# Kernel optimization log

Hardware: AMD Instinct MI355X
Metric: run time of the kernel (lower is better)

The kernel has to match this reference:

```python
import jax, jax.numpy as jnp
import numpy as np

BITS = 4
PACK = 32 // BITS  # 8 nibbles per int32
GROUPSIZE = 128
IN_F, OUT_F = 4096, 11008
N_GROUPS = IN_F // GROUPSIZE


def setup_inputs() -> dict:
    key = jax.random.key(0)
    k1, k2, k3, k4, k5 = jax.random.split(key, 5)
    x = jax.random.normal(k1, (8192, IN_F), dtype=jnp.float32)
    # packed int4 weights: 8 values per int32 along the infeatures axis
    qweight = jax.random.randint(k2, (IN_F // PACK, OUT_F), jnp.iinfo(jnp.int32).min,
                                 jnp.iinfo(jnp.int32).max, dtype=jnp.int32)
    # packed int4 zero points: 8 values per int32 along the outfeatures axis
    qzeros = jax.random.randint(k3, (N_GROUPS, OUT_F // PACK), jnp.iinfo(jnp.int32).min,
                                jnp.iinfo(jnp.int32).max, dtype=jnp.int32)
    # small positive per-group scales, as produced by GPTQ quantization
    scales = (jax.random.uniform(k4, (N_GROUPS, OUT_F), dtype=jnp.float32) * 0.01 + 0.001)
    g_idx = (jnp.arange(IN_F, dtype=jnp.int32) // GROUPSIZE).astype(jnp.int32)
    bias = jax.random.normal(k5, (OUT_F,), dtype=jnp.float32)
    return {"x": x, "qweight": qweight, "qzeros": qzeros, "scales": scales,
            "g_idx": g_idx, "bias": bias}


def _unpack_int4_rows(packed):
    # packed: [in/8, out] int32 -> [in, out] int32 nibbles
    shifts = (BITS * jnp.arange(PACK, dtype=jnp.int32))  # [8]
    nib = (packed[:, None, :] >> shifts[None, :, None]) & 0xF  # [in/8, 8, out]
    return nib.reshape(packed.shape[0] * PACK, packed.shape[1])


def _unpack_int4_cols(packed):
    # packed: [G, out/8] int32 -> [G, out] int32 nibbles
    shifts = (BITS * jnp.arange(PACK, dtype=jnp.int32))  # [8]
    nib = (packed[:, :, None] >> shifts[None, None, :]) & 0xF  # [G, out/8, 8]
    return nib.reshape(packed.shape[0], packed.shape[1] * PACK)


def reference(x, qweight, qzeros, scales, g_idx, bias):
    q = _unpack_int4_rows(qweight)            # [in, out] int4 values in [0,15]
    z = _unpack_int4_cols(qzeros) + 1         # pack() stored zeros-1; GPTQ dequant adds it back
    # per-input-channel group lookup via g_idx
    s = scales[g_idx]                         # [in, out]
    zf = z[g_idx].astype(jnp.float32)         # [in, out]
    w = (q.astype(jnp.float32) - zf) * s      # dequantized weight [in, out]
    out = jnp.matmul(x, w) + bias             # [tokens, out]
    return out
```

## Files before the change

### kernel.cpp

```cpp
#include <hip/hip_runtime.h>
#include <stdint.h>

#define TOKENS 8192
#define IN_F   4096
#define OUT_F  11008
#define GROUPSIZE 128

#define BM 256
#define BN 256
#define BK 64
#define NT  (IN_F / BK)
#define NBM (TOKENS / BM)
#define NBN (OUT_F / BN)
#define NWG (NBM * NBN)

typedef __attribute__((ext_vector_type(8)))  short          bf16x8;
typedef __attribute__((ext_vector_type(4)))  float          f32x4;
typedef __attribute__((ext_vector_type(8)))  unsigned short u16x8;
typedef __attribute__((ext_vector_type(16))) unsigned short u16x16;

static __device__ __forceinline__ unsigned short f2bf(float f) {
    union { float f; unsigned int u; } v; v.f = f;
    unsigned int u = v.u;
    u += 0x7fffu + ((u >> 16) & 1u);
    return (unsigned short)(u >> 16);
}

__global__ void cvt_x_kernel(const float* __restrict__ x,
                             unsigned short* __restrict__ xb) {
    int i = (blockIdx.x * 256 + threadIdx.x) * 8;
    const float4* p = (const float4*)(x + i);
    float4 a = p[0];
    float4 b = p[1];
    u16x8 o;
    o[0] = f2bf(a.x); o[1] = f2bf(a.y); o[2] = f2bf(a.z); o[3] = f2bf(a.w);
    o[4] = f2bf(b.x); o[5] = f2bf(b.y); o[6] = f2bf(b.z); o[7] = f2bf(b.w);
    *(u16x8*)(xb + i) = o;
}

__global__ void dequant_kernel(const int* __restrict__ qweight,
                               const int* __restrict__ qzeros,
                               const float* __restrict__ scales,
                               unsigned short* __restrict__ Wt) {
    const int t   = threadIdx.x;
    const int n   = blockIdx.x * 32 + (t >> 3);
    const int kp0 = blockIdx.y * 16 + (t & 7) * 2;
    const int g   = blockIdx.y;
    const float s  = scales[g * OUT_F + n];
    const int   zq = ((qzeros[g * (OUT_F / 8) + (n >> 3)] >> (4 * (n & 7))) & 0xF) + 1;
    const float zs = (float)zq * s;
    const int qw0 = qweight[(size_t)kp0 * OUT_F + n];
    const int qw1 = qweight[(size_t)(kp0 + 1) * OUT_F + n];
    u16x16 o;
#pragma unroll
    for (int j = 0; j < 8; ++j) {
        o[j]     = f2bf(fmaf((float)((qw0 >> (4 * j)) & 0xF), s, -zs));
        o[j + 8] = f2bf(fmaf((float)((qw1 >> (4 * j)) & 0xF), s, -zs));
    }
    *(u16x16*)(Wt + (size_t)n * IN_F + kp0 * 8) = o;
}

#define GLD16(gp, lp)                                                        \
    __builtin_amdgcn_global_load_lds(                                        \
        (const __attribute__((address_space(1))) unsigned int*)(gp),         \
        (__attribute__((address_space(3))) unsigned int*)(lp), 16, 0, 0)

#define BARRIER() do {                                                       \
    asm volatile("" ::: "memory");                                           \
    __builtin_amdgcn_s_barrier();                                            \
    asm volatile("" ::: "memory");                                           \
} while (0)

#define LGKM0() do {                                                         \
    asm volatile("s_waitcnt lgkmcnt(0)" ::: "memory");                       \
    __builtin_amdgcn_sched_barrier(0);                                       \
} while (0)

__global__ __launch_bounds__(512, 2) void gemm_bias_kernel(
    const unsigned short* __restrict__ A,
    const unsigned short* __restrict__ Bt,
    const float* __restrict__ bias,
    float* __restrict__ C) {
    extern __shared__ char smem_c[];

    const int tid = threadIdx.x;
    const int l   = tid & 63;
    const int w   = tid >> 6;
    const int wr  = w >> 2;
    const int wc  = w & 3;

    const int bid = blockIdx.x;
    const int swz = (bid & 7) * (NWG / 8) + (bid >> 3);
    const int m0  = (swz / NBN) * BM;
    const int n0  = (swz % NBN) * BN;

    const int sperm = ((l & 7) ^ (l >> 3)) * 8;
    const unsigned short* aG = A  + (size_t)(m0 + w * 16 + (l >> 3)) * IN_F + sperm;
    const unsigned short* bG = Bt + (size_t)(n0 + w * 16 + (l >> 3)) * IN_F + sperm;
    char* sA = smem_c + w * 2048 + l * 16;
    char* sB = sA + 32768;

#define STAGE_A(b, h, tt) do {                                               \
    GLD16(aG + (size_t)((h) * 128    ) * IN_F + (tt) * 64,                   \
          sA + (b) * 65536 + (h) * 16384);                                   \
    GLD16(aG + (size_t)((h) * 128 + 8) * IN_F + (tt) * 64,                   \
          sA + (b) * 65536 + (h) * 16384 + 1024);                            \
} while (0)
#define STAGE_B(b, h, tt) do {                                               \
    GLD16(bG + (size_t)((h) * 128    ) * IN_F + (tt) * 64,                   \
          sB + (b) * 65536 + (h) * 16384);                                   \
    GLD16(bG + (size_t)((h) * 128 + 8) * IN_F + (tt) * 64,                   \
          sB + (b) * 65536 + (h) * 16384 + 1024);                            \
} while (0)

    const unsigned short* LAe = (const unsigned short*)smem_c;
    const unsigned short* LBe = (const unsigned short*)(smem_c + 32768);
    const int c0   = (((l >> 4) ^ (l & 7)) * 8);
    const int c1   = c0 ^ 32;
    const int arow = (wr * 128 + (l & 15)) * 64;
    const int brow = (wc * 64  + (l & 15)) * 64;

    f32x4  acc[8][4] = {};
    bf16x8 a0[2], a1[2], bfr[4][2];

#define RDA_PAIR(p, mi) do {                                                 \
    a0[0] = *(const bf16x8*)&(p)[arow + (mi) * 1024 + c0];                   \
    a0[1] = *(const bf16x8*)&(p)[arow + (mi) * 1024 + c1];                   \
    a1[0] = *(const bf16x8*)&(p)[arow + ((mi) + 1) * 1024 + c0];             \
    a1[1] = *(const bf16x8*)&(p)[arow + ((mi) + 1) * 1024 + c1];             \
} while (0)
#define RDB(p, nj) do {                                                      \
    bfr[nj][0] = *(const bf16x8*)&(p)[brow + (nj) * 1024 + c0];              \
    bfr[nj][1] = *(const bf16x8*)&(p)[brow + (nj) * 1024 + c1];              \
} while (0)
#define MM0(mi, nj, ks)                                                      \
    acc[mi][nj] = __builtin_amdgcn_mfma_f32_16x16x32_bf16(                   \
        a0[ks], bfr[nj][ks], acc[mi][nj], 0, 0, 0)
#define MM1(mi, nj, ks)                                                      \
    acc[mi][nj] = __builtin_amdgcn_mfma_f32_16x16x32_bf16(                   \
        a1[ks], bfr[nj][ks], acc[mi][nj], 0, 0, 0)
#define QUADP(e) do {                                                        \
    __builtin_amdgcn_s_setprio(1);                                           \
    MM0(e,0,0); MM0(e,1,0); MM0(e,2,0); MM0(e,3,0);                          \
    MM1((e)+1,0,0); MM1((e)+1,1,0); MM1((e)+1,2,0); MM1((e)+1,3,0);          \
    MM0(e,0,1); MM0(e,1,1); MM0(e,2,1); MM0(e,3,1);                          \
    MM1((e)+1,0,1); MM1((e)+1,1,1); MM1((e)+1,2,1); MM1((e)+1,3,1);          \
    __builtin_amdgcn_s_setprio(0);                                           \
} while (0)

    STAGE_A(0, 0, 0); STAGE_A(0, 1, 0);
    STAGE_B(0, 0, 0); STAGE_B(0, 1, 0);
    STAGE_B(1, 0, 1); STAGE_B(1, 1, 1);
    asm volatile("s_waitcnt vmcnt(4)" ::: "memory");
    __builtin_amdgcn_sched_barrier(0);
    BARRIER();

    for (int t = 0; t < NT; ++t) {
        const int bt = t & 1;
        const int bo = bt ^ 1;
        const unsigned short* pA = LAe + bt * 32768;
        const unsigned short* pB = LBe + bt * 32768;

        RDB(pB, 0); RDB(pB, 1); RDB(pB, 2); RDB(pB, 3);
        RDA_PAIR(pA, 0);
        if (t + 1 < NT) STAGE_A(bo, 0, t + 1);
        BARRIER();
        LGKM0();
        QUADP(0);
        BARRIER();

        RDA_PAIR(pA, 2);
        if (t + 1 < NT) STAGE_A(bo, 1, t + 1);
        BARRIER();
        LGKM0();
        QUADP(2);
        BARRIER();

        RDA_PAIR(pA, 4);
        if (t + 2 < NT) STAGE_B(bt, 0, t + 2);
        BARRIER();
        LGKM0();
        QUADP(4);
        BARRIER();

        RDA_PAIR(pA, 6);
        if (t + 2 < NT) STAGE_B(bt, 1, t + 2);
        BARRIER();
        LGKM0();
        QUADP(6);
        if (t < NT - 2)
            asm volatile("s_waitcnt vmcnt(4)" ::: "memory");
        else if (t == NT - 2)
            asm volatile("s_waitcnt vmcnt(0)" ::: "memory");
        __builtin_amdgcn_sched_barrier(0);
        BARRIER();
    }

    const int col = l & 15;
    const int r0  = (l >> 4) * 4;
#pragma unroll
    for (int nj = 0; nj < 4; ++nj) {
        const int n = n0 + wc * 64 + nj * 16 + col;
        const float bv = bias[n];
#pragma unroll
        for (int mi = 0; mi < 8; ++mi) {
            const int m = m0 + wr * 128 + mi * 16 + r0;
#pragma unroll
            for (int r = 0; r < 4; ++r)
                C[(size_t)(m + r) * OUT_F + n] = acc[mi][nj][r] + bv;
        }
    }
}

__global__ __launch_bounds__(256) void fallback_kernel(
    const float* __restrict__ x, const int* __restrict__ qweight,
    const int* __restrict__ qzeros, const float* __restrict__ scales,
    const float* __restrict__ bias, float* __restrict__ C) {
    const int n = blockIdx.x * 16 + (threadIdx.x & 15);
    const int m = blockIdx.y * 16 + (threadIdx.x >> 4);
    float acc = 0.f;
    const float* xr = x + (size_t)m * IN_F;
    for (int g = 0; g < IN_F / GROUPSIZE; ++g) {
        const float s  = scales[g * OUT_F + n];
        const float zs = s * (float)(((qzeros[g * (OUT_F / 8) + (n >> 3)]
                                       >> (4 * (n & 7))) & 0xF) + 1);
        for (int kp = g * 16; kp < g * 16 + 16; ++kp) {
            const int qw = qweight[kp * OUT_F + n];
#pragma unroll
            for (int j = 0; j < 8; ++j) {
                const float w = fmaf((float)((qw >> (4 * j)) & 0xF), s, -zs);
                acc = fmaf(xr[kp * 8 + j], w, acc);
            }
        }
    }
    C[(size_t)m * OUT_F + n] = acc + bias[n];
}

extern "C" void kernel_launch(void* const* d_in, const int* in_sizes, int n_in,
                              void* d_out, int out_size, void* d_ws, size_t ws_size,
                              hipStream_t stream) {
    const float* x       = (const float*)d_in[0];
    const int*   qweight = (const int*)  d_in[1];
    const int*   qzeros  = (const int*)  d_in[2];
    const float* scales  = (const float*)d_in[3];
    const float* bias    = (const float*)d_in[5];
    float* out = (float*)d_out;

    const size_t xb_bytes = (size_t)TOKENS * IN_F * sizeof(unsigned short);
    const size_t wt_bytes = (size_t)OUT_F  * IN_F * sizeof(unsigned short);

    if (ws_size >= xb_bytes + wt_bytes) {
        static bool attr_done = false;
        if (!attr_done) {
            (void)hipFuncSetAttribute((const void*)gemm_bias_kernel,
                                      hipFuncAttributeMaxDynamicSharedMemorySize,
                                      131072);
            attr_done = true;
        }
        unsigned short* xb = (unsigned short*)d_ws;
        unsigned short* Wt = (unsigned short*)((char*)d_ws + xb_bytes);
        cvt_x_kernel<<<(TOKENS * IN_F) / (256 * 8), 256, 0, stream>>>(x, xb);
        dequant_kernel<<<dim3(OUT_F / 32, IN_F / 8 / 16), 256, 0, stream>>>(
            qweight, qzeros, scales, Wt);
        gemm_bias_kernel<<<NWG, 512, 131072, stream>>>(xb, Wt, bias, out);
    } else {
        fallback_kernel<<<dim3(OUT_F / 16, TOKENS / 16), 256, 0, stream>>>(
            x, qweight, qzeros, scales, bias, out);
    }
}
```

Measured before the change: 1.080 ms.

## Triple-buffer A tiles and restructure GEMM main loop with partial LDS waits

```diff
diff --git a/kernel.cpp b/kernel.cpp
--- a/kernel.cpp
+++ b/kernel.cpp
@@ -71,8 +71,8 @@
     asm volatile("" ::: "memory");                                           \
 } while (0)
 
-#define LGKM0() do {                                                         \
-    asm volatile("s_waitcnt lgkmcnt(0)" ::: "memory");                       \
+#define LGKM(n) do {                                                         \
+    asm volatile("s_waitcnt lgkmcnt(" #n ")" ::: "memory");                  \
     __builtin_amdgcn_sched_barrier(0);                                       \
 } while (0)
 
@@ -97,103 +97,95 @@
     const int sperm = ((l & 7) ^ (l >> 3)) * 8;
     const unsigned short* aG = A  + (size_t)(m0 + w * 16 + (l >> 3)) * IN_F + sperm;
     const unsigned short* bG = Bt + (size_t)(n0 + w * 16 + (l >> 3)) * IN_F + sperm;
-    char* sA = smem_c + w * 2048 + l * 16;
-    char* sB = sA + 32768;
-
-#define STAGE_A(b, h, tt) do {                                               \
-    GLD16(aG + (size_t)((h) * 128    ) * IN_F + (tt) * 64,                   \
-          sA + (b) * 65536 + (h) * 16384);                                   \
-    GLD16(aG + (size_t)((h) * 128 + 8) * IN_F + (tt) * 64,                   \
-          sA + (b) * 65536 + (h) * 16384 + 1024);                            \
-} while (0)
-#define STAGE_B(b, h, tt) do {                                               \
-    GLD16(bG + (size_t)((h) * 128    ) * IN_F + (tt) * 64,                   \
-          sB + (b) * 65536 + (h) * 16384);                                   \
-    GLD16(bG + (size_t)((h) * 128 + 8) * IN_F + (tt) * 64,                   \
-          sB + (b) * 65536 + (h) * 16384 + 1024);                            \
-} while (0)
-
-    const unsigned short* LAe = (const unsigned short*)smem_c;
-    const unsigned short* LBe = (const unsigned short*)(smem_c + 32768);
+    const int sOff = w * 2048 + l * 16;
+
+#define STAGE_A4(lbase, tt) do {                                             \
+    GLD16(aG + (size_t)(tt) * 64,                      (lbase) + sOff);      \
+    GLD16(aG + (size_t)8   * IN_F + (size_t)(tt) * 64, (lbase) + sOff + 1024);\
+    GLD16(aG + (size_t)128 * IN_F + (size_t)(tt) * 64, (lbase) + sOff + 16384);\
+    GLD16(aG + (size_t)136 * IN_F + (size_t)(tt) * 64, (lbase) + sOff + 16384 + 1024);\
+} while (0)
+#define STAGE_B4(lbase, tt) do {                                             \
+    GLD16(bG + (size_t)(tt) * 64,                      (lbase) + sOff);      \
+    GLD16(bG + (size_t)8   * IN_F + (size_t)(tt) * 64, (lbase) + sOff + 1024);\
+    GLD16(bG + (size_t)128 * IN_F + (size_t)(tt) * 64, (lbase) + sOff + 16384);\
+    GLD16(bG + (size_t)136 * IN_F + (size_t)(tt) * 64, (lbase) + sOff + 16384 + 1024);\
+} while (0)
+
     const int c0   = (((l >> 4) ^ (l & 7)) * 8);
     const int c1   = c0 ^ 32;
     const int arow = (wr * 128 + (l & 15)) * 64;
     const int brow = (wc * 64  + (l & 15)) * 64;
 
     f32x4  acc[8][4] = {};
-    bf16x8 a0[2], a1[2], bfr[4][2];
-
-#define RDA_PAIR(p, mi) do {                                                 \
-    a0[0] = *(const bf16x8*)&(p)[arow + (mi) * 1024 + c0];                   \
-    a0[1] = *(const bf16x8*)&(p)[arow + (mi) * 1024 + c1];                   \
-    a1[0] = *(const bf16x8*)&(p)[arow + ((mi) + 1) * 1024 + c0];             \
-    a1[1] = *(const bf16x8*)&(p)[arow + ((mi) + 1) * 1024 + c1];             \
-} while (0)
-#define RDB(p, nj) do {                                                      \
-    bfr[nj][0] = *(const bf16x8*)&(p)[brow + (nj) * 1024 + c0];              \
-    bfr[nj][1] = *(const bf16x8*)&(p)[brow + (nj) * 1024 + c1];              \
-} while (0)
-#define MM0(mi, nj, ks)                                                      \
+    bf16x8 aP0[2], aP1[2], aQ0[2], aQ1[2], bfr[4][2];
+
+#define RDB4(p) do {                                                         \
+    bfr[0][0] = *(const bf16x8*)&(p)[brow + 0 * 1024 + c0];                  \
+    bfr[0][1] = *(const bf16x8*)&(p)[brow + 0 * 1024 + c1];                  \
+    bfr[1][0] = *(const bf16x8*)&(p)[brow + 1 * 1024 + c0];                  \
+    bfr[1][1] = *(const bf16x8*)&(p)[brow + 1 * 1024 + c1];                  \
+    bfr[2][0] = *(const bf16x8*)&(p)[brow + 2 * 1024 + c0];                  \
+    bfr[2][1] = *(const bf16x8*)&(p)[brow + 2 * 1024 + c1];                  \
+    bfr[3][0] = *(const bf16x8*)&(p)[brow + 3 * 1024 + c0];                  \
+    bfr[3][1] = *(const bf16x8*)&(p)[brow + 3 * 1024 + c1];                  \
+} while (0)
+#define RDA2(p, mi, d0, d1) do {                                             \
+    d0[0] = *(const bf16x8*)&(p)[arow + (mi) * 1024 + c0];                   \
+    d0[1] = *(const bf16x8*)&(p)[arow + (mi) * 1024 + c1];                   \
+    d1[0] = *(const bf16x8*)&(p)[arow + ((mi) + 1) * 1024 + c0];             \
+    d1[1] = *(const bf16x8*)&(p)[arow + ((mi) + 1) * 1024 + c1];             \
+} while (0)
+#define MMX(Af, mi, nj, ks)                                                  \
     acc[mi][nj] = __builtin_amdgcn_mfma_f32_16x16x32_bf16(                   \
-        a0[ks], bfr[nj][ks], acc[mi][nj], 0, 0, 0)
-#define MM1(mi, nj, ks)                                                      \
-    acc[mi][nj] = __builtin_amdgcn_mfma_f32_16x16x32_bf16(                   \
-        a1[ks], bfr[nj][ks], acc[mi][nj], 0, 0, 0)
-#define QUADP(e) do {                                                        \
+        Af[ks], bfr[nj][ks], acc[mi][nj], 0, 0, 0)
+#define QUADX(A0, A1, e) do {                                                \
     __builtin_amdgcn_s_setprio(1);                                           \
-    MM0(e,0,0); MM0(e,1,0); MM0(e,2,0); MM0(e,3,0);                          \
-    MM1((e)+1,0,0); MM1((e)+1,1,0); MM1((e)+1,2,0); MM1((e)+1,3,0);          \
-    MM0(e,0,1); MM0(e,1,1); MM0(e,2,1); MM0(e,3,1);                          \
-    MM1((e)+1,0,1); MM1((e)+1,1,1); MM1((e)+1,2,1); MM1((e)+1,3,1);          \
+    MMX(A0, e, 0, 0); MMX(A0, e, 1, 0); MMX(A0, e, 2, 0); MMX(A0, e, 3, 0);  \
+    MMX(A1, (e)+1, 0, 0); MMX(A1, (e)+1, 1, 0); MMX(A1, (e)+1, 2, 0); MMX(A1, (e)+1, 3, 0); \
+    MMX(A0, e, 0, 1); MMX(A0, e, 1, 1); MMX(A0, e, 2, 1); MMX(A0, e, 3, 1);  \
+    MMX(A1, (e)+1, 0, 1); MMX(A1, (e)+1, 1, 1); MMX(A1, (e)+1, 2, 1); MMX(A1, (e)+1, 3, 1); \
     __builtin_amdgcn_s_setprio(0);                                           \
 } while (0)
 
-    STAGE_A(0, 0, 0); STAGE_A(0, 1, 0);
-    STAGE_B(0, 0, 0); STAGE_B(0, 1, 0);
-    STAGE_B(1, 0, 1); STAGE_B(1, 1, 1);
-    asm volatile("s_waitcnt vmcnt(4)" ::: "memory");
+    int aOff0 = 0, aOff1 = 32768, aOff2 = 65536;
+    int bOff0 = 98304, bOff1 = 131072;
+
+    STAGE_A4(smem_c + aOff0, 0); STAGE_B4(smem_c + bOff0, 0);
+    STAGE_A4(smem_c + aOff1, 1); STAGE_B4(smem_c + bOff1, 1);
+    asm volatile("s_waitcnt vmcnt(8)" ::: "memory");
     __builtin_amdgcn_sched_barrier(0);
     BARRIER();
 
+#pragma unroll 1
     for (int t = 0; t < NT; ++t) {
-        const int bt = t & 1;
-        const int bo = bt ^ 1;
-        const unsigned short* pA = LAe + bt * 32768;
-        const unsigned short* pB = LBe + bt * 32768;
-
-        RDB(pB, 0); RDB(pB, 1); RDB(pB, 2); RDB(pB, 3);
-        RDA_PAIR(pA, 0);
-        if (t + 1 < NT) STAGE_A(bo, 0, t + 1);
+        const unsigned short* pA = (const unsigned short*)(smem_c + aOff0);
+        const unsigned short* pB = (const unsigned short*)(smem_c + bOff0);
+
+        RDB4(pB);
+        if (t + 2 < NT) STAGE_A4(smem_c + aOff2, t + 2);
+        LGKM(0);
         BARRIER();
-        LGKM0();
-        QUADP(0);
-        BARRIER();
-
-        RDA_PAIR(pA, 2);
-        if (t + 1 < NT) STAGE_A(bo, 1, t + 1);
-        BARRIER();
-        LGKM0();
-        QUADP(2);
-        BARRIER();
-
-        RDA_PAIR(pA, 4);
-        if (t + 2 < NT) STAGE_B(bt, 0, t + 2);
-        BARRIER();
-        LGKM0();
-        QUADP(4);
-        BARRIER();
-
-        RDA_PAIR(pA, 6);
-        if (t + 2 < NT) STAGE_B(bt, 1, t + 2);
-        BARRIER();
-        LGKM0();
-        QUADP(6);
+        if (t + 2 < NT) STAGE_B4(smem_c + bOff0, t + 2);
+
+        RDA2(pA, 0, aP0, aP1);
+        RDA2(pA, 2, aQ0, aQ1);
+        LGKM(4);  QUADX(aP0, aP1, 0);
+        RDA2(pA, 4, aP0, aP1);
+        LGKM(4);  QUADX(aQ0, aQ1, 2);
+        RDA2(pA, 6, aQ0, aQ1);
+        LGKM(4);  QUADX(aP0, aP1, 4);
+        LGKM(0);  QUADX(aQ0, aQ1, 6);
+
         if (t < NT - 2)
-            asm volatile("s_waitcnt vmcnt(4)" ::: "memory");
-        else if (t == NT - 2)
+            asm volatile("s_waitcnt vmcnt(8)" ::: "memory");
+        else
             asm volatile("s_waitcnt vmcnt(0)" ::: "memory");
         __builtin_amdgcn_sched_barrier(0);
         BARRIER();
+
+        int ta = aOff0; aOff0 = aOff1; aOff1 = aOff2; aOff2 = ta;
+        int tb = bOff0; bOff0 = bOff1; bOff1 = tb;
     }
 
     const int col = l & 15;
@@ -207,7 +199,8 @@
             const int m = m0 + wr * 128 + mi * 16 + r0;
 #pragma unroll
             for (int r = 0; r < 4; ++r)
-                C[(size_t)(m + r) * OUT_F + n] = acc[mi][nj][r] + bv;
+                __builtin_nontemporal_store(acc[mi][nj][r] + bv,
+                                            &C[(size_t)(m + r) * OUT_F + n]);
         }
     }
 }
@@ -249,20 +242,21 @@
     const size_t xb_bytes = (size_t)TOKENS * IN_F * sizeof(unsigned short);
     const size_t wt_bytes = (size_t)OUT_F  * IN_F * sizeof(unsigned short);
 
-    if (ws_size >= xb_bytes + wt_bytes) {
-        static bool attr_done = false;
-        if (!attr_done) {
-            (void)hipFuncSetAttribute((const void*)gemm_bias_kernel,
-                                      hipFuncAttributeMaxDynamicSharedMemorySize,
-                                      131072);
-            attr_done = true;
-        }
+    static int lds_ok = -1;
+    if (lds_ok < 0) {
+        hipError_t e = hipFuncSetAttribute((const void*)gemm_bias_kernel,
+                                           hipFuncAttributeMaxDynamicSharedMemorySize,
+                                           163840);
+        lds_ok = (e == hipSuccess) ? 1 : 0;
+    }
+
+    if (ws_size >= xb_bytes + wt_bytes && lds_ok == 1) {
         unsigned short* xb = (unsigned short*)d_ws;
         unsigned short* Wt = (unsigned short*)((char*)d_ws + xb_bytes);
         cvt_x_kernel<<<(TOKENS * IN_F) / (256 * 8), 256, 0, stream>>>(x, xb);
         dequant_kernel<<<dim3(OUT_F / 32, IN_F / 8 / 16), 256, 0, stream>>>(
             qweight, qzeros, scales, Wt);
-        gemm_bias_kernel<<<NWG, 512, 131072, stream>>>(xb, Wt, bias, out);
+        gemm_bias_kernel<<<NWG, 512, 163840, stream>>>(xb, Wt, bias, out);
     } else {
         fallback_kernel<<<dim3(OUT_F / 16, TOKENS / 16), 256, 0, stream>>>(
             x, qweight, qzeros, scales, bias, out);
```

Result: slower. 1.119 ms (+3.6%).
